# Kernel optimization log

Measured on AMD Instinct MI355X. Metric: run time of the kernel, lower is better.

## Reference

```python
import jax, jax.numpy as jnp
import numpy as np

N_NODES = 50000
N_EDGES = 1250000
D = 64


def setup_inputs() -> dict:
    key = jax.random.key(0)
    ks = jax.random.split(key, 9)
    s = 1.0 / np.sqrt(D)
    return {
        "y": jax.random.normal(ks[0], (N_NODES, D), dtype=jnp.float32),
        "src": jax.random.randint(ks[1], (N_EDGES,), 0, N_NODES, dtype=jnp.int32),
        "dst": jax.random.randint(ks[2], (N_EDGES,), 0, N_NODES, dtype=jnp.int32),
        "W1": jax.random.normal(ks[3], (D, D), dtype=jnp.float32) * s,
        "b1": jnp.zeros((D,), dtype=jnp.float32),
        "W2": jax.random.normal(ks[4], (D, D), dtype=jnp.float32) * s,
        "b2": jnp.zeros((D,), dtype=jnp.float32),
        "U1": jax.random.normal(ks[5], (D, D), dtype=jnp.float32) * s,
        "c1": jnp.zeros((D,), dtype=jnp.float32),
        "U2": jax.random.normal(ks[6], (D, D), dtype=jnp.float32) * s,
        "c2": jnp.zeros((D,), dtype=jnp.float32),
    }


def reference(y, src, dst, W1, b1, W2, b2, U1, c1, U2, c2):
    # msg = relu(FNN_pre(y[src])) ; FNN = Linear -> ReLU -> Linear
    xs = y[src]                                        # [E, D] gather
    h1 = jax.nn.relu(xs @ W1 + b1)                     # [E, D]
    msg = jax.nn.relu(h1 @ W2 + b2)                    # [E, D]
    # z = segment-sum of messages at destination nodes
    z = jax.ops.segment_sum(msg, dst, num_segments=N_NODES)  # [N, D]
    # h = relu(FNN_update(z))
    h2 = jax.nn.relu(z @ U1 + c1)                      # [N, D]
    h = jax.nn.relu(h2 @ U2 + c2)                      # [N, D]
    return h
```

## Files before the change

kernel.cpp:

```cpp
#include <hip/hip_runtime.h>

#define D 64
#define CHUNK 4096
#define BSHIFT 8
#define MAXB 8192

typedef unsigned int uint;
typedef unsigned short ushort;

using bf16x8 = __attribute__((ext_vector_type(8))) short;
using f32x4  = __attribute__((ext_vector_type(4))) float;

__device__ __forceinline__ uint f2bf(float f) {
    uint u = __float_as_uint(f);
    return (u + 0x7fffu + ((u >> 16) & 1u)) >> 16;
}
__device__ __forceinline__ uint pk2(float a, float b) {
    return f2bf(a) | (f2bf(b) << 16);
}

#define ACC8M(v, aE, aO, mk) do {                                              \
    aE[0] = fmaf(mk, __uint_as_float((v).x << 16), aE[0]);                     \
    aO[0] = fmaf(mk, __uint_as_float((v).x & 0xffff0000u), aO[0]);             \
    aE[1] = fmaf(mk, __uint_as_float((v).y << 16), aE[1]);                     \
    aO[1] = fmaf(mk, __uint_as_float((v).y & 0xffff0000u), aO[1]);             \
    aE[2] = fmaf(mk, __uint_as_float((v).z << 16), aE[2]);                     \
    aO[2] = fmaf(mk, __uint_as_float((v).z & 0xffff0000u), aO[2]);             \
    aE[3] = fmaf(mk, __uint_as_float((v).w << 16), aE[3]);                     \
    aO[3] = fmaf(mk, __uint_as_float((v).w & 0xffff0000u), aO[3]);             \
} while (0)

template <bool BF16IN, bool BF16OUT>
__device__ __forceinline__ void mlp_tile(
    int tile, ushort (*Hs)[72],
    const float* __restrict__ Xf, const ushort* __restrict__ Xb,
    const ushort* __restrict__ pkW1, const float* __restrict__ b1v,
    const ushort* __restrict__ pkW2, const float* __restrict__ b2v,
    ushort* __restrict__ out16, float* __restrict__ out32, int N)
{
    const int lane = threadIdx.x & 63;
    const int m = lane & 15;
    const int q = lane >> 4;

    bf16x8 w1f[4][2], w2f[4][2];
    #pragma unroll
    for (int t = 0; t < 4; ++t) {
        #pragma unroll
        for (int kf = 0; kf < 2; ++kf) {
            const int off = ((t * 2 + kf) * 64 + lane) << 3;
            w1f[t][kf] = *(const bf16x8*)(pkW1 + off);
            w2f[t][kf] = *(const bf16x8*)(pkW2 + off);
        }
    }

    const int rowbase = tile * 16;
    int r = rowbase + m;
    if (r >= N) r = N - 1;
    bf16x8 ax0, ax1;
    if (BF16IN) {
        const ushort* xr = Xb + (size_t)r * D + q * 8;
        ax0 = *(const bf16x8*)xr;
        ax1 = *(const bf16x8*)(xr + 32);
    } else {
        const float* xr = Xf + (size_t)r * D + q * 8;
        float4 x0 = *(const float4*)xr;
        float4 x1 = *(const float4*)(xr + 4);
        float4 x2 = *(const float4*)(xr + 32);
        float4 x3 = *(const float4*)(xr + 36);
        ax0[0]=(short)f2bf(x0.x); ax0[1]=(short)f2bf(x0.y);
        ax0[2]=(short)f2bf(x0.z); ax0[3]=(short)f2bf(x0.w);
        ax0[4]=(short)f2bf(x1.x); ax0[5]=(short)f2bf(x1.y);
        ax0[6]=(short)f2bf(x1.z); ax0[7]=(short)f2bf(x1.w);
        ax1[0]=(short)f2bf(x2.x); ax1[1]=(short)f2bf(x2.y);
        ax1[2]=(short)f2bf(x2.z); ax1[3]=(short)f2bf(x2.w);
        ax1[4]=(short)f2bf(x3.x); ax1[5]=(short)f2bf(x3.y);
        ax1[6]=(short)f2bf(x3.z); ax1[7]=(short)f2bf(x3.w);
    }

    const f32x4 zero4 = {0.f, 0.f, 0.f, 0.f};
    f32x4 acc[4];

    #pragma unroll
    for (int t = 0; t < 4; ++t) acc[t] = zero4;
    #pragma unroll
    for (int t = 0; t < 4; ++t) {
        acc[t] = __builtin_amdgcn_mfma_f32_16x16x32_bf16(ax0, w1f[t][0], acc[t], 0, 0, 0);
        acc[t] = __builtin_amdgcn_mfma_f32_16x16x32_bf16(ax1, w1f[t][1], acc[t], 0, 0, 0);
    }
    #pragma unroll
    for (int t = 0; t < 4; ++t) {
        const float bv = b1v[t * 16 + m];
        #pragma unroll
        for (int rg = 0; rg < 4; ++rg) {
            float hv = fmaxf(acc[t][rg] + bv, 0.f);
            Hs[q * 4 + rg][t * 16 + m] = (ushort)f2bf(hv);
        }
    }
    __syncthreads();

    bf16x8 ah0 = *(const bf16x8*)&Hs[m][q * 8];
    bf16x8 ah1 = *(const bf16x8*)&Hs[m][32 + q * 8];

    #pragma unroll
    for (int t = 0; t < 4; ++t) acc[t] = zero4;
    #pragma unroll
    for (int t = 0; t < 4; ++t) {
        acc[t] = __builtin_amdgcn_mfma_f32_16x16x32_bf16(ah0, w2f[t][0], acc[t], 0, 0, 0);
        acc[t] = __builtin_amdgcn_mfma_f32_16x16x32_bf16(ah1, w2f[t][1], acc[t], 0, 0, 0);
    }
    #pragma unroll
    for (int t = 0; t < 4; ++t) {
        const float bv = b2v[t * 16 + m];
        #pragma unroll
        for (int rg = 0; rg < 4; ++rg) {
            const int row = rowbase + q * 4 + rg;
            if (row < N) {
                float ov = fmaxf(acc[t][rg] + bv, 0.f);
                if (BF16OUT) out16[(size_t)row * D + t * 16 + m] = (ushort)f2bf(ov);
                else         out32[(size_t)row * D + t * 16 + m] = ov;
            }
        }
    }
}

__global__ __launch_bounds__(256) void kA_hist_pack(
    const int* __restrict__ dst, int* __restrict__ histG, int E, int NBA,
    const float* __restrict__ W1, const float* __restrict__ W2,
    const float* __restrict__ U1, const float* __restrict__ U2,
    ushort* __restrict__ pkAll)
{
    __shared__ int lhist[256];
    const int t = threadIdx.x;
    if ((int)blockIdx.x < NBA) {
        lhist[t] = 0;
        __syncthreads();
        const int cbase = blockIdx.x * CHUNK;
        const int lim = min(CHUNK, E - cbase);
        if (lim == CHUNK) {
            const int4* dp = (const int4*)(dst + cbase);
            int4 d4[4];
            #pragma unroll
            for (int g = 0; g < 4; ++g) d4[g] = dp[g * 256 + t];
            #pragma unroll
            for (int g = 0; g < 4; ++g) {
                atomicAdd(&lhist[(uint)d4[g].x >> BSHIFT], 1);
                atomicAdd(&lhist[(uint)d4[g].y >> BSHIFT], 1);
                atomicAdd(&lhist[(uint)d4[g].z >> BSHIFT], 1);
                atomicAdd(&lhist[(uint)d4[g].w >> BSHIFT], 1);
            }
        } else {
            for (int j = t; j < lim; j += 256)
                atomicAdd(&lhist[(uint)dst[cbase + j] >> BSHIFT], 1);
        }
        __syncthreads();
        histG[blockIdx.x * 256 + t] = lhist[t];
    } else {
        const int mtx = blockIdx.x - NBA;
        const float* W = (mtx == 0) ? W1 : (mtx == 1) ? W2 : (mtx == 2) ? U1 : U2;
        ushort* pk = pkAll + mtx * 4096;
        for (int u = t; u < 512; u += 256) {
            const int t_ = u >> 7;
            const int rem = u & 127;
            const int kf = rem >> 6;
            const int lane = rem & 63;
            const int q = lane >> 4, m = lane & 15;
            const int n = t_ * 16 + m;
            uint w[4];
            #pragma unroll
            for (int j2 = 0; j2 < 4; ++j2) {
                const int k = kf * 32 + q * 8 + 2 * j2;
                w[j2] = pk2(W[k * D + n], W[(k + 1) * D + n]);
            }
            uint4 v = { w[0], w[1], w[2], w[3] };
            *(uint4*)(pk + (u << 3)) = v;
        }
    }
}

__global__ __launch_bounds__(256) void kB_scan(
    const int* __restrict__ histG, int* __restrict__ startG,
    int* __restrict__ tot, int NBA)
{
    __shared__ int tmp[256];
    const int t = threadIdx.x;
    const int b = blockIdx.x;
    const int K = (NBA + 255) / 256;
    const int c0 = t * K;
    int loc[8];
    int s = 0;
    #pragma unroll
    for (int i = 0; i < 8; ++i) {
        if (i < K) {
            const int c = c0 + i;
            loc[i] = s;
            s += (c < NBA) ? histG[c * 256 + b] : 0;
        }
    }
    int x = s; tmp[t] = x; __syncthreads();
    #pragma unroll
    for (int off = 1; off < 256; off <<= 1) {
        int add = (t >= off) ? tmp[t - off] : 0; __syncthreads();
        x += add; tmp[t] = x; __syncthreads();
    }
    const int base = x - s;
    #pragma unroll
    for (int i = 0; i < 8; ++i) {
        if (i < K) {
            const int c = c0 + i;
            if (c < NBA) startG[c * 256 + b] = base + loc[i];
        }
    }
    if (t == 255) tot[b] = x;
}

__global__ __launch_bounds__(256) void kC_part_mlp1(
    const int* __restrict__ src, const int* __restrict__ dst,
    const int* __restrict__ startG, const int* __restrict__ tot,
    uint* __restrict__ packedG, int E, int NBA,
    const float* __restrict__ y, const ushort* __restrict__ pkAll,
    const float* __restrict__ b1, const float* __restrict__ b2,
    ushort* __restrict__ msg16, int N)
{
    __shared__ int t1[256];
    __shared__ int cur[256];
    __shared__ __align__(16) ushort Hs[4][16][72];
    const int t = threadIdx.x;
    if ((int)blockIdx.x < NBA) {
        int tv = tot[t];
        int x = tv; t1[t] = x; __syncthreads();
        #pragma unroll
        for (int off = 1; off < 256; off <<= 1) {
            int add = (t >= off) ? t1[t - off] : 0; __syncthreads();
            x += add; t1[t] = x; __syncthreads();
        }
        cur[t] = (x - tv) + startG[blockIdx.x * 256 + t];
        __syncthreads();
        const int cbase = blockIdx.x * CHUNK;
        const int lim = min(CHUNK, E - cbase);
        if (lim == CHUNK) {
            const int4* sp = (const int4*)(src + cbase);
            const int4* dp = (const int4*)(dst + cbase);
            int4 s4[4], d4[4];
            #pragma unroll
            for (int g = 0; g < 4; ++g) { s4[g] = sp[g * 256 + t]; d4[g] = dp[g * 256 + t]; }
            #pragma unroll
            for (int g = 0; g < 4; ++g) {
                int pos;
                pos = atomicAdd(&cur[(uint)d4[g].x >> BSHIFT], 1);
                packedG[pos] = ((uint)(d4[g].x & 255) << 16) | (uint)s4[g].x;
                pos = atomicAdd(&cur[(uint)d4[g].y >> BSHIFT], 1);
                packedG[pos] = ((uint)(d4[g].y & 255) << 16) | (uint)s4[g].y;
                pos = atomicAdd(&cur[(uint)d4[g].z >> BSHIFT], 1);
                packedG[pos] = ((uint)(d4[g].z & 255) << 16) | (uint)s4[g].z;
                pos = atomicAdd(&cur[(uint)d4[g].w >> BSHIFT], 1);
                packedG[pos] = ((uint)(d4[g].w & 255) << 16) | (uint)s4[g].w;
            }
        } else {
            for (int j = t; j < lim; j += 256) {
                const int e = cbase + j;
                int s = src[e], d = dst[e];
                int pos = atomicAdd(&cur[(uint)d >> BSHIFT], 1);
                packedG[pos] = ((uint)(d & 255) << 16) | (uint)s;
            }
        }
    } else {
        const int tile = (blockIdx.x - NBA) * 4 + (t >> 6);
        mlp_tile<false, true>(tile, Hs[t >> 6], y, nullptr,
                              pkAll + 0 * 4096, b1, pkAll + 1 * 4096, b2,
                              msg16, nullptr, N);
    }
}

__global__ __launch_bounds__(256) void kF_place(
    const uint* __restrict__ packedG, const int* __restrict__ tot,
    ushort* __restrict__ sortedG, int* __restrict__ offsets, int N, int E)
{
    __shared__ int t1[256];
    __shared__ int cnt[256];
    __shared__ int cur[256];
    __shared__ uint pk[MAXB];
    __shared__ ushort srt[MAXB];
    const int t = threadIdx.x;
    const int b = blockIdx.x;

    int tv = tot[t];
    int x = tv; t1[t] = x; __syncthreads();
    #pragma unroll
    for (int off = 1; off < 256; off <<= 1) {
        int add = (t >= off) ? t1[t - off] : 0; __syncthreads();
        x += add; t1[t] = x; __syncthreads();
    }
    const int pbase = (b == 0) ? 0 : t1[b - 1];
    const int cn = tot[b];
    const bool fits = (cn <= MAXB);

    cnt[t] = 0;
    __syncthreads();
    if (fits) {
        for (int i = t; i < cn; i += 256) pk[i] = packedG[pbase + i];
        __syncthreads();
        for (int i = t; i < cn; i += 256) atomicAdd(&cnt[pk[i] >> 16], 1);
    } else {
        for (int i = t; i < cn; i += 256)
            atomicAdd(&cnt[packedG[pbase + i] >> 16], 1);
    }
    __syncthreads();

    int c = cnt[t];
    int x2 = c; t1[t] = x2; __syncthreads();
    #pragma unroll
    for (int off = 1; off < 256; off <<= 1) {
        int add = (t >= off) ? t1[t - off] : 0; __syncthreads();
        x2 += add; t1[t] = x2; __syncthreads();
    }
    const int excl = x2 - c;
    const int node = b * 256 + t;
    if (node < N) offsets[node] = pbase + excl;
    if (b == 0 && t == 0) offsets[N] = E;

    if (fits) {
        cur[t] = excl;
        __syncthreads();
        for (int i = t; i < cn; i += 256) {
            uint e = pk[i];
            int p = atomicAdd(&cur[e >> 16], 1);
            srt[p] = (ushort)(e & 0xffffu);
        }
        __syncthreads();
        for (int i = t; i < cn; i += 256)
            sortedG[pbase + i] = srt[i];
    } else {
        cur[t] = pbase + excl;
        __syncthreads();
        for (int i = t; i < cn; i += 256) {
            uint e = packedG[pbase + i];
            int p = atomicAdd(&cur[e >> 16], 1);
            sortedG[p] = (ushort)(e & 0xffffu);
        }
    }
}

__global__ __launch_bounds__(256, 6) void k5_gather(
    const ushort* __restrict__ msg16,
    const int* __restrict__ offsets, const ushort* __restrict__ sortedG,
    ushort* __restrict__ z16, int n_nodes)
{
    const int lane = threadIdx.x & 63;
    const int sub = lane & 7;
    const int grp = (lane >> 3) & 3;
    const int half = lane >> 5;
    const int p = blockIdx.x * 4 + (threadIdx.x >> 6);
    if (p * 2 >= n_nodes) return;
    const ushort* mbase = msg16 + (sub << 3);

    const int n = 2 * p + half;
    const bool nvalid = n < n_nodes;
    int beg = 0, end = 0;
    if (nvalid) { beg = offsets[n]; end = offsets[n + 1]; }
    const int m = end - beg;
    const int m0 = __builtin_amdgcn_readfirstlane(m);
    const int m1 = __builtin_amdgcn_readlane(m, 32);
    const int mmax = max(m0, m1);

    float aE[4] = {0, 0, 0, 0}, aO[4] = {0, 0, 0, 0};

    for (int base = 0; base < mmax; base += 32) {
        int s[8];
        float mk[8];
        #pragma unroll
        for (int j = 0; j < 8; ++j) {
            if (base + j * 4 < mmax) {
                const int e = base + j * 4 + grp;
                const bool on = (e < m);
                mk[j] = on ? 1.f : 0.f;
                s[j] = (int)sortedG[on ? (beg + e) : 0];
            }
        }
        uint4 v[8];
        #pragma unroll
        for (int j = 0; j < 8; ++j)
            if (base + j * 4 < mmax)
                v[j] = *(const uint4*)(mbase + ((size_t)s[j] << 6));
        #pragma unroll
        for (int j = 0; j < 8; ++j)
            if (base + j * 4 < mmax) { ACC8M(v[j], aE, aO, mk[j]); }
    }

    #pragma unroll
    for (int d2 = 0; d2 < 4; ++d2) {
        aE[d2] += __shfl_xor(aE[d2], 8, 64);
        aO[d2] += __shfl_xor(aO[d2], 8, 64);
        aE[d2] += __shfl_xor(aE[d2], 16, 64);
        aO[d2] += __shfl_xor(aO[d2], 16, 64);
    }
    if (grp == 0 && nvalid) {
        uint4 pv;
        pv.x = pk2(aE[0], aO[0]);
        pv.y = pk2(aE[1], aO[1]);
        pv.z = pk2(aE[2], aO[2]);
        pv.w = pk2(aE[3], aO[3]);
        *(uint4*)(z16 + (size_t)n * D + (sub << 3)) = pv;
    }
}

__global__ __launch_bounds__(256) void k_mlp2(
    const ushort* __restrict__ z16, const ushort* __restrict__ pkAll,
    const float* __restrict__ c1, const float* __restrict__ c2,
    float* __restrict__ out, int N)
{
    __shared__ __align__(16) ushort Hs[4][16][72];
    const int tile = blockIdx.x * 4 + (threadIdx.x >> 6);
    mlp_tile<true, false>(tile, Hs[threadIdx.x >> 6], nullptr, z16,
                          pkAll + 2 * 4096, c1, pkAll + 3 * 4096, c2,
                          nullptr, out, N);
}

extern "C" void kernel_launch(void* const* d_in, const int* in_sizes, int n_in,
                              void* d_out, int out_size, void* d_ws, size_t ws_size,
                              hipStream_t stream) {
    const float* y  = (const float*)d_in[0];
    const int*  src = (const int*) d_in[1];
    const int*  dst = (const int*) d_in[2];
    const float* W1 = (const float*)d_in[3];
    const float* b1 = (const float*)d_in[4];
    const float* W2 = (const float*)d_in[5];
    const float* b2 = (const float*)d_in[6];
    const float* U1 = (const float*)d_in[7];
    const float* c1 = (const float*)d_in[8];
    const float* U2 = (const float*)d_in[9];
    const float* c2 = (const float*)d_in[10];

    const int N = in_sizes[0] / D;
    const int E = in_sizes[1];
    const int NBA   = (E + CHUNK - 1) / CHUNK;
    const int NBUCK = (N + 255) / 256;
    const int NT    = (N + 15) / 16;
    const int MB    = (NT + 3) / 4;
    const int G5    = (N / 2 + 3) / 4;

    char* ws = (char*)d_ws;
    auto al16 = [](size_t x) { return (x + 15) & ~15ull; };
    ushort* msg16   = (ushort*)ws;  ws += al16((size_t)N * D * 2);
    int*    offsets = (int*)ws;     ws += al16((size_t)(N + 1) * 4);
    int*    tot     = (int*)ws;     ws += al16(256 * 4);
    ushort* sortedG = (ushort*)ws;  ws += al16((size_t)E * 2);
    ushort* pkAll   = (ushort*)ws;  ws += al16(4 * 4096 * 2);
    ushort* z16     = (ushort*)ws;
    int*    histG   = (int*)ws;
    int*    startG  = histG + (size_t)NBA * 256;
    uint*   packedG = (uint*)(startG + (size_t)NBA * 256);

    kA_hist_pack<<<NBA + 4, 256, 0, stream>>>(
        dst, histG, E, NBA, W1, W2, U1, U2, pkAll);

    kB_scan<<<NBUCK > 256 ? NBUCK : 256, 256, 0, stream>>>(histG, startG, tot, NBA);

    kC_part_mlp1<<<NBA + MB, 256, 0, stream>>>(
        src, dst, startG, tot, packedG, E, NBA,
        y, pkAll, b1, b2, msg16, N);

    kF_place<<<NBUCK, 256, 0, stream>>>(packedG, tot, sortedG, offsets, N, E);

    k5_gather<<<G5, 256, 0, stream>>>(msg16, offsets, sortedG, z16, N);

    k_mlp2<<<MB, 256, 0, stream>>>(z16, pkAll, c1, c2, (float*)d_out, N);
}
```

Before: 141.0 us.

## Fuse bucket placement, gather-sum and update MLP into one kernel with 64-node buckets

Shrinks the destination buckets from 256 to 64 nodes, so there are 1024 buckets. The old place, gather and update-MLP kernels become one kernel. Each block sorts its bucket's edges locally in shared memory, accumulates the messages per node in fp32, and runs the update MLP straight from shared memory. This removes the global sortedG, offsets and z16 round trips and two kernel launches. In exchange, each lane handles one node with 4 lanes per node, which can cause imbalance from the per-wave max-degree loop, and the histogram and scan arrays grow fourfold.

```diff
diff --git a/kernel.cpp b/kernel.cpp
--- a/kernel.cpp
+++ b/kernel.cpp
@@ -2,8 +2,9 @@
 
 #define D 64
 #define CHUNK 4096
-#define BSHIFT 8
-#define MAXB 8192
+#define BSHIFT 6
+#define NB 1024
+#define GCH 4096
 
 typedef unsigned int uint;
 typedef unsigned short ushort;
@@ -30,51 +31,27 @@
     aO[3] = fmaf(mk, __uint_as_float((v).w & 0xffff0000u), aO[3]);             \
 } while (0)
 
-template <bool BF16IN, bool BF16OUT>
-__device__ __forceinline__ void mlp_tile(
-    int tile, ushort (*Hs)[72],
-    const float* __restrict__ Xf, const ushort* __restrict__ Xb,
-    const ushort* __restrict__ pkW1, const float* __restrict__ b1v,
-    const ushort* __restrict__ pkW2, const float* __restrict__ b2v,
-    ushort* __restrict__ out16, float* __restrict__ out32, int N)
+template <bool BF16OUT>
+__device__ __forceinline__ void mlp_from_frags(
+    bf16x8 ax0, bf16x8 ax1, ushort (*Hs)[72],
+    const ushort* __restrict__ pkWa, const float* __restrict__ bav,
+    const ushort* __restrict__ pkWb, const float* __restrict__ bbv,
+    ushort* __restrict__ out16, float* __restrict__ out32,
+    int rowbase, int N)
 {
     const int lane = threadIdx.x & 63;
     const int m = lane & 15;
     const int q = lane >> 4;
 
-    bf16x8 w1f[4][2], w2f[4][2];
+    bf16x8 waf[4][2], wbf[4][2];
     #pragma unroll
     for (int t = 0; t < 4; ++t) {
         #pragma unroll
         for (int kf = 0; kf < 2; ++kf) {
             const int off = ((t * 2 + kf) * 64 + lane) << 3;
-            w1f[t][kf] = *(const bf16x8*)(pkW1 + off);
-            w2f[t][kf] = *(const bf16x8*)(pkW2 + off);
-        }
-    }
-
-    const int rowbase = tile * 16;
-    int r = rowbase + m;
-    if (r >= N) r = N - 1;
-    bf16x8 ax0, ax1;
-    if (BF16IN) {
-        const ushort* xr = Xb + (size_t)r * D + q * 8;
-        ax0 = *(const bf16x8*)xr;
-        ax1 = *(const bf16x8*)(xr + 32);
-    } else {
-        const float* xr = Xf + (size_t)r * D + q * 8;
-        float4 x0 = *(const float4*)xr;
-        float4 x1 = *(const float4*)(xr + 4);
-        float4 x2 = *(const float4*)(xr + 32);
-        float4 x3 = *(const float4*)(xr + 36);
-        ax0[0]=(short)f2bf(x0.x); ax0[1]=(short)f2bf(x0.y);
-        ax0[2]=(short)f2bf(x0.z); ax0[3]=(short)f2bf(x0.w);
-        ax0[4]=(short)f2bf(x1.x); ax0[5]=(short)f2bf(x1.y);
-        ax0[6]=(short)f2bf(x1.z); ax0[7]=(short)f2bf(x1.w);
-        ax1[0]=(short)f2bf(x2.x); ax1[1]=(short)f2bf(x2.y);
-        ax1[2]=(short)f2bf(x2.z); ax1[3]=(short)f2bf(x2.w);
-        ax1[4]=(short)f2bf(x3.x); ax1[5]=(short)f2bf(x3.y);
-        ax1[6]=(short)f2bf(x3.z); ax1[7]=(short)f2bf(x3.w);
+            waf[t][kf] = *(const bf16x8*)(pkWa + off);
+            wbf[t][kf] = *(const bf16x8*)(pkWb + off);
+        }
     }
 
     const f32x4 zero4 = {0.f, 0.f, 0.f, 0.f};
@@ -84,12 +61,12 @@
     for (int t = 0; t < 4; ++t) acc[t] = zero4;
     #pragma unroll
     for (int t = 0; t < 4; ++t) {
-        acc[t] = __builtin_amdgcn_mfma_f32_16x16x32_bf16(ax0, w1f[t][0], acc[t], 0, 0, 0);
-        acc[t] = __builtin_amdgcn_mfma_f32_16x16x32_bf16(ax1, w1f[t][1], acc[t], 0, 0, 0);
+        acc[t] = __builtin_amdgcn_mfma_f32_16x16x32_bf16(ax0, waf[t][0], acc[t], 0, 0, 0);
+        acc[t] = __builtin_amdgcn_mfma_f32_16x16x32_bf16(ax1, waf[t][1], acc[t], 0, 0, 0);
     }
     #pragma unroll
     for (int t = 0; t < 4; ++t) {
-        const float bv = b1v[t * 16 + m];
+        const float bv = bav[t * 16 + m];
         #pragma unroll
         for (int rg = 0; rg < 4; ++rg) {
             float hv = fmaxf(acc[t][rg] + bv, 0.f);
@@ -105,12 +82,12 @@
     for (int t = 0; t < 4; ++t) acc[t] = zero4;
     #pragma unroll
     for (int t = 0; t < 4; ++t) {
-        acc[t] = __builtin_amdgcn_mfma_f32_16x16x32_bf16(ah0, w2f[t][0], acc[t], 0, 0, 0);
-        acc[t] = __builtin_amdgcn_mfma_f32_16x16x32_bf16(ah1, w2f[t][1], acc[t], 0, 0, 0);
+        acc[t] = __builtin_amdgcn_mfma_f32_16x16x32_bf16(ah0, wbf[t][0], acc[t], 0, 0, 0);
+        acc[t] = __builtin_amdgcn_mfma_f32_16x16x32_bf16(ah1, wbf[t][1], acc[t], 0, 0, 0);
     }
     #pragma unroll
     for (int t = 0; t < 4; ++t) {
-        const float bv = b2v[t * 16 + m];
+        const float bv = bbv[t * 16 + m];
         #pragma unroll
         for (int rg = 0; rg < 4; ++rg) {
             const int row = rowbase + q * 4 + rg;
@@ -123,16 +100,47 @@
     }
 }
 
+__device__ __forceinline__ void mlp_msg_tile(
+    int tile, ushort (*Hs)[72], const float* __restrict__ Xf,
+    const ushort* __restrict__ pkW1, const float* __restrict__ b1v,
+    const ushort* __restrict__ pkW2, const float* __restrict__ b2v,
+    ushort* __restrict__ msg16, int N)
+{
+    const int lane = threadIdx.x & 63;
+    const int m = lane & 15;
+    const int q = lane >> 4;
+    const int rowbase = tile * 16;
+    int r = rowbase + m;
+    if (r >= N) r = N - 1;
+    const float* xr = Xf + (size_t)r * D + q * 8;
+    float4 x0 = *(const float4*)xr;
+    float4 x1 = *(const float4*)(xr + 4);
+    float4 x2 = *(const float4*)(xr + 32);
+    float4 x3 = *(const float4*)(xr + 36);
+    bf16x8 ax0, ax1;
+    ax0[0]=(short)f2bf(x0.x); ax0[1]=(short)f2bf(x0.y);
+    ax0[2]=(short)f2bf(x0.z); ax0[3]=(short)f2bf(x0.w);
+    ax0[4]=(short)f2bf(x1.x); ax0[5]=(short)f2bf(x1.y);
+    ax0[6]=(short)f2bf(x1.z); ax0[7]=(short)f2bf(x1.w);
+    ax1[0]=(short)f2bf(x2.x); ax1[1]=(short)f2bf(x2.y);
+    ax1[2]=(short)f2bf(x2.z); ax1[3]=(short)f2bf(x2.w);
+    ax1[4]=(short)f2bf(x3.x); ax1[5]=(short)f2bf(x3.y);
+    ax1[6]=(short)f2bf(x3.z); ax1[7]=(short)f2bf(x3.w);
+    mlp_from_frags<true>(ax0, ax1, Hs, pkW1, b1v, pkW2, b2v,
+                         msg16, nullptr, rowbase, N);
+}
+
 __global__ __launch_bounds__(256) void kA_hist_pack(
     const int* __restrict__ dst, int* __restrict__ histG, int E, int NBA,
     const float* __restrict__ W1, const float* __restrict__ W2,
     const float* __restrict__ U1, const float* __restrict__ U2,
     ushort* __restrict__ pkAll)
 {
-    __shared__ int lhist[256];
+    __shared__ int lhist[NB];
     const int t = threadIdx.x;
     if ((int)blockIdx.x < NBA) {
-        lhist[t] = 0;
+        #pragma unroll
+        for (int i = t; i < NB; i += 256) lhist[i] = 0;
         __syncthreads();
         const int cbase = blockIdx.x * CHUNK;
         const int lim = min(CHUNK, E - cbase);
@@ -153,7 +161,8 @@
                 atomicAdd(&lhist[(uint)dst[cbase + j] >> BSHIFT], 1);
         }
         __syncthreads();
-        histG[blockIdx.x * 256 + t] = lhist[t];
+        for (int i = t; i < NB; i += 256)
+            histG[blockIdx.x * NB + i] = lhist[i];
     } else {
         const int mtx = blockIdx.x - NBA;
         const float* W = (mtx == 0) ? W1 : (mtx == 1) ? W2 : (mtx == 2) ? U1 : U2;
@@ -193,7 +202,7 @@
         if (i < K) {
             const int c = c0 + i;
             loc[i] = s;
-            s += (c < NBA) ? histG[c * 256 + b] : 0;
+            s += (c < NBA) ? histG[c * NB + b] : 0;
         }
     }
     int x = s; tmp[t] = x; __syncthreads();
@@ -207,7 +216,7 @@
     for (int i = 0; i < 8; ++i) {
         if (i < K) {
             const int c = c0 + i;
-            if (c < NBA) startG[c * 256 + b] = base + loc[i];
+            if (c < NBA) startG[c * NB + b] = base + loc[i];
         }
     }
     if (t == 255) tot[b] = x;
@@ -216,24 +225,38 @@
 __global__ __launch_bounds__(256) void kC_part_mlp1(
     const int* __restrict__ src, const int* __restrict__ dst,
     const int* __restrict__ startG, const int* __restrict__ tot,
-    uint* __restrict__ packedG, int E, int NBA,
+    uint* __restrict__ packedG, int* __restrict__ bbase, int E, int NBA,
     const float* __restrict__ y, const ushort* __restrict__ pkAll,
     const float* __restrict__ b1, const float* __restrict__ b2,
     ushort* __restrict__ msg16, int N)
 {
-    __shared__ int t1[256];
-    __shared__ int cur[256];
+    __shared__ int tmp[256];
+    __shared__ int cur[NB];
     __shared__ __align__(16) ushort Hs[4][16][72];
     const int t = threadIdx.x;
     if ((int)blockIdx.x < NBA) {
-        int tv = tot[t];
-        int x = tv; t1[t] = x; __syncthreads();
+        const int t4 = t << 2;
+        const int tv0 = tot[t4], tv1 = tot[t4 + 1];
+        const int tv2 = tot[t4 + 2], tv3 = tot[t4 + 3];
+        const int ss = tv0 + tv1 + tv2 + tv3;
+        int x = ss; tmp[t] = x; __syncthreads();
         #pragma unroll
         for (int off = 1; off < 256; off <<= 1) {
-            int add = (t >= off) ? t1[t - off] : 0; __syncthreads();
-            x += add; t1[t] = x; __syncthreads();
-        }
-        cur[t] = (x - tv) + startG[blockIdx.x * 256 + t];
+            int add = (t >= off) ? tmp[t - off] : 0; __syncthreads();
+            x += add; tmp[t] = x; __syncthreads();
+        }
+        const int e0 = x - ss;
+        const int sb = blockIdx.x * NB;
+        cur[t4]     = e0 + startG[sb + t4];
+        cur[t4 + 1] = e0 + tv0 + startG[sb + t4 + 1];
+        cur[t4 + 2] = e0 + tv0 + tv1 + startG[sb + t4 + 2];
+        cur[t4 + 3] = e0 + tv0 + tv1 + tv2 + startG[sb + t4 + 3];
+        if (blockIdx.x == 0) {
+            bbase[t4]     = e0;
+            bbase[t4 + 1] = e0 + tv0;
+            bbase[t4 + 2] = e0 + tv0 + tv1;
+            bbase[t4 + 3] = e0 + tv0 + tv1 + tv2;
+        }
         __syncthreads();
         const int cbase = blockIdx.x * CHUNK;
         const int lim = min(CHUNK, E - cbase);
@@ -247,172 +270,143 @@
             for (int g = 0; g < 4; ++g) {
                 int pos;
                 pos = atomicAdd(&cur[(uint)d4[g].x >> BSHIFT], 1);
-                packedG[pos] = ((uint)(d4[g].x & 255) << 16) | (uint)s4[g].x;
+                packedG[pos] = ((uint)(d4[g].x & 63) << 16) | (uint)s4[g].x;
                 pos = atomicAdd(&cur[(uint)d4[g].y >> BSHIFT], 1);
-                packedG[pos] = ((uint)(d4[g].y & 255) << 16) | (uint)s4[g].y;
+                packedG[pos] = ((uint)(d4[g].y & 63) << 16) | (uint)s4[g].y;
                 pos = atomicAdd(&cur[(uint)d4[g].z >> BSHIFT], 1);
-                packedG[pos] = ((uint)(d4[g].z & 255) << 16) | (uint)s4[g].z;
+                packedG[pos] = ((uint)(d4[g].z & 63) << 16) | (uint)s4[g].z;
                 pos = atomicAdd(&cur[(uint)d4[g].w >> BSHIFT], 1);
-                packedG[pos] = ((uint)(d4[g].w & 255) << 16) | (uint)s4[g].w;
+                packedG[pos] = ((uint)(d4[g].w & 63) << 16) | (uint)s4[g].w;
             }
         } else {
             for (int j = t; j < lim; j += 256) {
                 const int e = cbase + j;
                 int s = src[e], d = dst[e];
                 int pos = atomicAdd(&cur[(uint)d >> BSHIFT], 1);
-                packedG[pos] = ((uint)(d & 255) << 16) | (uint)s;
+                packedG[pos] = ((uint)(d & 63) << 16) | (uint)s;
             }
         }
     } else {
         const int tile = (blockIdx.x - NBA) * 4 + (t >> 6);
-        mlp_tile<false, true>(tile, Hs[t >> 6], y, nullptr,
-                              pkAll + 0 * 4096, b1, pkAll + 1 * 4096, b2,
-                              msg16, nullptr, N);
-    }
-}
-
-__global__ __launch_bounds__(256) void kF_place(
-    const uint* __restrict__ packedG, const int* __restrict__ tot,
-    ushort* __restrict__ sortedG, int* __restrict__ offsets, int N, int E)
-{
-    __shared__ int t1[256];
-    __shared__ int cnt[256];
-    __shared__ int cur[256];
-    __shared__ uint pk[MAXB];
-    __shared__ ushort srt[MAXB];
+        mlp_msg_tile(tile, Hs[t >> 6], y,
+                     pkAll + 0 * 4096, b1, pkAll + 1 * 4096, b2, msg16, N);
+    }
+}
+
+__global__ __launch_bounds__(256, 4) void kG_fused(
+    const uint* __restrict__ packedG, const int* __restrict__ bbase,
+    const int* __restrict__ tot, const ushort* __restrict__ msg16,
+    const ushort* __restrict__ pkAll, const float* __restrict__ c1,
+    const float* __restrict__ c2, float* __restrict__ out, int N)
+{
+    __shared__ int cnt[64], excl[64], cur[64];
+    __shared__ ushort srt[GCH];
+    __shared__ __align__(16) float zt[64][68];
+    __shared__ __align__(16) ushort Hs[4][16][72];
+
     const int t = threadIdx.x;
     const int b = blockIdx.x;
-
-    int tv = tot[t];
-    int x = tv; t1[t] = x; __syncthreads();
-    #pragma unroll
-    for (int off = 1; off < 256; off <<= 1) {
-        int add = (t >= off) ? t1[t - off] : 0; __syncthreads();
-        x += add; t1[t] = x; __syncthreads();
-    }
-    const int pbase = (b == 0) ? 0 : t1[b - 1];
+    const int pbase = bbase[b];
     const int cn = tot[b];
-    const bool fits = (cn <= MAXB);
-
-    cnt[t] = 0;
-    __syncthreads();
-    if (fits) {
-        for (int i = t; i < cn; i += 256) pk[i] = packedG[pbase + i];
-        __syncthreads();
-        for (int i = t; i < cn; i += 256) atomicAdd(&cnt[pk[i] >> 16], 1);
-    } else {
-        for (int i = t; i < cn; i += 256)
-            atomicAdd(&cnt[packedG[pbase + i] >> 16], 1);
-    }
-    __syncthreads();
-
-    int c = cnt[t];
-    int x2 = c; t1[t] = x2; __syncthreads();
-    #pragma unroll
-    for (int off = 1; off < 256; off <<= 1) {
-        int add = (t >= off) ? t1[t - off] : 0; __syncthreads();
-        x2 += add; t1[t] = x2; __syncthreads();
-    }
-    const int excl = x2 - c;
-    const int node = b * 256 + t;
-    if (node < N) offsets[node] = pbase + excl;
-    if (b == 0 && t == 0) offsets[N] = E;
-
-    if (fits) {
-        cur[t] = excl;
-        __syncthreads();
-        for (int i = t; i < cn; i += 256) {
-            uint e = pk[i];
+    const int lane = t & 63;
+    const int w = t >> 6;
+    const int nl = w * 16 + (lane >> 2);
+    const int lsub = lane & 3;
+    const ushort* mb = msg16 + (lsub << 4);
+
+    float aE[8] = {0, 0, 0, 0, 0, 0, 0, 0};
+    float aO[8] = {0, 0, 0, 0, 0, 0, 0, 0};
+
+    for (int base = 0; base < cn; base += GCH) {
+        const int lim = min(GCH, cn - base);
+        if (t < 64) cnt[t] = 0;
+        __syncthreads();
+        for (int i = t; i < lim; i += 256)
+            atomicAdd(&cnt[packedG[pbase + base + i] >> 16], 1);
+        __syncthreads();
+        if (t < 64) {
+            int c = cnt[t];
+            int x = c;
+            #pragma unroll
+            for (int off = 1; off < 64; off <<= 1) {
+                int yv = __shfl_up(x, off, 64);
+                if (lane >= off) x += yv;
+            }
+            excl[t] = x - c;
+            cur[t] = x - c;
+        }
+        __syncthreads();
+        for (int i = t; i < lim; i += 256) {
+            uint e = packedG[pbase + base + i];
             int p = atomicAdd(&cur[e >> 16], 1);
             srt[p] = (ushort)(e & 0xffffu);
         }
         __syncthreads();
-        for (int i = t; i < cn; i += 256)
-            sortedG[pbase + i] = srt[i];
-    } else {
-        cur[t] = pbase + excl;
-        __syncthreads();
-        for (int i = t; i < cn; i += 256) {
-            uint e = packedG[pbase + i];
-            int p = atomicAdd(&cur[e >> 16], 1);
-            sortedG[p] = (ushort)(e & 0xffffu);
-        }
-    }
-}
-
-__global__ __launch_bounds__(256, 6) void k5_gather(
-    const ushort* __restrict__ msg16,
-    const int* __restrict__ offsets, const ushort* __restrict__ sortedG,
-    ushort* __restrict__ z16, int n_nodes)
-{
-    const int lane = threadIdx.x & 63;
-    const int sub = lane & 7;
-    const int grp = (lane >> 3) & 3;
-    const int half = lane >> 5;
-    const int p = blockIdx.x * 4 + (threadIdx.x >> 6);
-    if (p * 2 >= n_nodes) return;
-    const ushort* mbase = msg16 + (sub << 3);
-
-    const int n = 2 * p + half;
-    const bool nvalid = n < n_nodes;
-    int beg = 0, end = 0;
-    if (nvalid) { beg = offsets[n]; end = offsets[n + 1]; }
-    const int m = end - beg;
-    const int m0 = __builtin_amdgcn_readfirstlane(m);
-    const int m1 = __builtin_amdgcn_readlane(m, 32);
-    const int mmax = max(m0, m1);
-
-    float aE[4] = {0, 0, 0, 0}, aO[4] = {0, 0, 0, 0};
-
-    for (int base = 0; base < mmax; base += 32) {
-        int s[8];
-        float mk[8];
-        #pragma unroll
-        for (int j = 0; j < 8; ++j) {
-            if (base + j * 4 < mmax) {
-                const int e = base + j * 4 + grp;
-                const bool on = (e < m);
+
+        const int deg = cnt[nl];
+        const int beg = excl[nl];
+        int mmax = deg;
+        #pragma unroll
+        for (int off = 4; off < 64; off <<= 1)
+            mmax = max(mmax, __shfl_xor(mmax, off, 64));
+        for (int e0 = 0; e0 < mmax; e0 += 4) {
+            int s[4];
+            float mk[4];
+            #pragma unroll
+            for (int j = 0; j < 4; ++j) {
+                const int e = e0 + j;
+                const bool on = e < deg;
                 mk[j] = on ? 1.f : 0.f;
-                s[j] = (int)sortedG[on ? (beg + e) : 0];
-            }
-        }
-        uint4 v[8];
-        #pragma unroll
-        for (int j = 0; j < 8; ++j)
-            if (base + j * 4 < mmax)
-                v[j] = *(const uint4*)(mbase + ((size_t)s[j] << 6));
-        #pragma unroll
-        for (int j = 0; j < 8; ++j)
-            if (base + j * 4 < mmax) { ACC8M(v[j], aE, aO, mk[j]); }
-    }
-
-    #pragma unroll
-    for (int d2 = 0; d2 < 4; ++d2) {
-        aE[d2] += __shfl_xor(aE[d2], 8, 64);
-        aO[d2] += __shfl_xor(aO[d2], 8, 64);
-        aE[d2] += __shfl_xor(aE[d2], 16, 64);
-        aO[d2] += __shfl_xor(aO[d2], 16, 64);
-    }
-    if (grp == 0 && nvalid) {
-        uint4 pv;
-        pv.x = pk2(aE[0], aO[0]);
-        pv.y = pk2(aE[1], aO[1]);
-        pv.z = pk2(aE[2], aO[2]);
-        pv.w = pk2(aE[3], aO[3]);
-        *(uint4*)(z16 + (size_t)n * D + (sub << 3)) = pv;
-    }
-}
-
-__global__ __launch_bounds__(256) void k_mlp2(
-    const ushort* __restrict__ z16, const ushort* __restrict__ pkAll,
-    const float* __restrict__ c1, const float* __restrict__ c2,
-    float* __restrict__ out, int N)
-{
-    __shared__ __align__(16) ushort Hs[4][16][72];
-    const int tile = blockIdx.x * 4 + (threadIdx.x >> 6);
-    mlp_tile<true, false>(tile, Hs[threadIdx.x >> 6], nullptr, z16,
+                s[j] = on ? (int)srt[beg + e] : 0;
+            }
+            uint4 v0[4], v1[4];
+            #pragma unroll
+            for (int j = 0; j < 4; ++j) {
+                const ushort* r = mb + ((size_t)s[j] << 6);
+                v0[j] = *(const uint4*)r;
+                v1[j] = *(const uint4*)(r + 8);
+            }
+            #pragma unroll
+            for (int j = 0; j < 4; ++j) {
+                ACC8M(v0[j], aE, aO, mk[j]);
+                ACC8M(v1[j], (aE + 4), (aO + 4), mk[j]);
+            }
+        }
+        __syncthreads();
+    }
+
+    {
+        const int c0 = lsub << 4;
+        float4 f0 = {aE[0], aO[0], aE[1], aO[1]};
+        float4 f1 = {aE[2], aO[2], aE[3], aO[3]};
+        float4 f2 = {aE[4], aO[4], aE[5], aO[5]};
+        float4 f3 = {aE[6], aO[6], aE[7], aO[7]};
+        *(float4*)&zt[nl][c0]      = f0;
+        *(float4*)&zt[nl][c0 + 4]  = f1;
+        *(float4*)&zt[nl][c0 + 8]  = f2;
+        *(float4*)&zt[nl][c0 + 12] = f3;
+    }
+    __syncthreads();
+
+    const int m = lane & 15;
+    const int q = lane >> 4;
+    const float* zr = &zt[w * 16 + m][q * 8];
+    float4 x0 = *(const float4*)zr;
+    float4 x1 = *(const float4*)(zr + 4);
+    float4 x2 = *(const float4*)(zr + 32);
+    float4 x3 = *(const float4*)(zr + 36);
+    bf16x8 ax0, ax1;
+    ax0[0]=(short)f2bf(x0.x); ax0[1]=(short)f2bf(x0.y);
+    ax0[2]=(short)f2bf(x0.z); ax0[3]=(short)f2bf(x0.w);
+    ax0[4]=(short)f2bf(x1.x); ax0[5]=(short)f2bf(x1.y);
+    ax0[6]=(short)f2bf(x1.z); ax0[7]=(short)f2bf(x1.w);
+    ax1[0]=(short)f2bf(x2.x); ax1[1]=(short)f2bf(x2.y);
+    ax1[2]=(short)f2bf(x2.z); ax1[3]=(short)f2bf(x2.w);
+    ax1[4]=(short)f2bf(x3.x); ax1[5]=(short)f2bf(x3.y);
+    ax1[6]=(short)f2bf(x3.z); ax1[7]=(short)f2bf(x3.w);
+    mlp_from_frags<false>(ax0, ax1, Hs[w],
                           pkAll + 2 * 4096, c1, pkAll + 3 * 4096, c2,
-                          nullptr, out, N);
+                          nullptr, out, b * 64 + w * 16, N);
 }
 
 extern "C" void kernel_launch(void* const* d_in, const int* in_sizes, int n_in,
@@ -432,36 +426,30 @@
 
     const int N = in_sizes[0] / D;
     const int E = in_sizes[1];
-    const int NBA   = (E + CHUNK - 1) / CHUNK;
-    const int NBUCK = (N + 255) / 256;
-    const int NT    = (N + 15) / 16;
-    const int MB    = (NT + 3) / 4;
-    const int G5    = (N / 2 + 3) / 4;
+    const int NBA = (E + CHUNK - 1) / CHUNK;
+    const int NT  = (N + 15) / 16;
+    const int MB  = (NT + 3) / 4;
+    const int NG  = (N + 63) >> 6;
 
     char* ws = (char*)d_ws;
     auto al16 = [](size_t x) { return (x + 15) & ~15ull; };
     ushort* msg16   = (ushort*)ws;  ws += al16((size_t)N * D * 2);
-    int*    offsets = (int*)ws;     ws += al16((size_t)(N + 1) * 4);
-    int*    tot     = (int*)ws;     ws += al16(256 * 4);
-    ushort* sortedG = (ushort*)ws;  ws += al16((size_t)E * 2);
     ushort* pkAll   = (ushort*)ws;  ws += al16(4 * 4096 * 2);
-    ushort* z16     = (ushort*)ws;
-    int*    histG   = (int*)ws;
-    int*    startG  = histG + (size_t)NBA * 256;
-    uint*   packedG = (uint*)(startG + (size_t)NBA * 256);
+    int*    tot     = (int*)ws;     ws += al16(NB * 4);
+    int*    bbase   = (int*)ws;     ws += al16(NB * 4);
+    int*    histG   = (int*)ws;     ws += al16((size_t)NBA * NB * 4);
+    int*    startG  = (int*)ws;     ws += al16((size_t)NBA * NB * 4);
+    uint*   packedG = (uint*)ws;    ws += al16((size_t)E * 4);
 
     kA_hist_pack<<<NBA + 4, 256, 0, stream>>>(
         dst, histG, E, NBA, W1, W2, U1, U2, pkAll);
 
-    kB_scan<<<NBUCK > 256 ? NBUCK : 256, 256, 0, stream>>>(histG, startG, tot, NBA);
+    kB_scan<<<NB, 256, 0, stream>>>(histG, startG, tot, NBA);
 
     kC_part_mlp1<<<NBA + MB, 256, 0, stream>>>(
-        src, dst, startG, tot, packedG, E, NBA,
+        src, dst, startG, tot, packedG, bbase, E, NBA,
         y, pkAll, b1, b2, msg16, N);
 
-    kF_place<<<NBUCK, 256, 0, stream>>>(packedG, tot, sortedG, offsets, N, E);
-
-    k5_gather<<<G5, 256, 0, stream>>>(msg16, offsets, sortedG, z16, N);
-
-    k_mlp2<<<MB, 256, 0, stream>>>(z16, pkAll, c1, c2, (float*)d_out, N);
-}
+    kG_fused<<<NG, 256, 0, stream>>>(
+        packedG, bbase, tot, msg16, pkAll, c1, c2, (float*)d_out, N);
+}
```

Result: no change. 139.7 us (-1.0%).
